# Optimization experiments

Hardware: AMD Instinct MI355X
Metric: run time of the kernel (lower is better)

Reference implementation:

```python
import jax, jax.numpy as jnp
import numpy as np

D_IN = 1024
D_OUT = 1024


def setup_inputs() -> dict:
    key = jax.random.key(0)
    ks = jax.random.split(key, 7)
    x = jax.random.normal(ks[0], (4, 2048, D_IN), dtype=jnp.float32)
    scale = 1.0 / np.sqrt(D_IN)
    Wq = jax.random.normal(ks[1], (D_IN, D_OUT), dtype=jnp.float32) * scale
    Wk = jax.random.normal(ks[2], (D_IN, D_OUT), dtype=jnp.float32) * scale
    Wv = jax.random.normal(ks[3], (D_IN, D_OUT), dtype=jnp.float32) * scale
    bq = jax.random.normal(ks[4], (D_OUT,), dtype=jnp.float32) * 0.01
    bk = jax.random.normal(ks[5], (D_OUT,), dtype=jnp.float32) * 0.01
    bv = jax.random.normal(ks[6], (D_OUT,), dtype=jnp.float32) * 0.01
    return {"x": x, "Wq": Wq, "bq": bq, "Wk": Wk, "bk": bk, "Wv": Wv, "bv": bv}


def reference(x, Wq, bq, Wk, bk, Wv, bv):
    # x: [B, S, d_in]
    q = jnp.einsum("bsd,de->bse", x, Wq) + bq  # [B, S, d_out]
    k = jnp.einsum("bsd,de->bse", x, Wk) + bk
    v = jnp.einsum("bsd,de->bse", x, Wv) + bv
    d_out = q.shape[-1]
    scores = jnp.einsum("bqe,bke->bqk", q, k) / jnp.sqrt(jnp.float32(d_out))
    attn = jax.nn.softmax(scores, axis=-1)  # [B, S, S]
    return jnp.einsum("bqk,bke->bqe", attn, v)
```

## Files before the change

### kernel.cpp

```cpp
#include <hip/hip_runtime.h>
#include <hip/hip_bf16.h>
#include <stdint.h>

typedef __bf16 bf16x8 __attribute__((ext_vector_type(8)));
typedef __bf16 bf16x4 __attribute__((ext_vector_type(4)));
typedef float f32x4 __attribute__((ext_vector_type(4)));

#define DEV __device__ __forceinline__

DEV void gload_lds16(const void* g, void* l) {
  __builtin_amdgcn_global_load_lds((const __attribute__((address_space(1))) void*)g,
                                   (__attribute__((address_space(3))) void*)l, 16, 0, 0);
}

#define WAITV(n) asm volatile("s_waitcnt vmcnt(" #n ")" ::: "memory")

__global__ __launch_bounds__(256) void pack_x_kernel(const float* __restrict__ x,
                                                     __bf16* __restrict__ o, long n) {
  long i = ((long)blockIdx.x * 256 + threadIdx.x) * 4;
  const long stride = (long)gridDim.x * 256 * 4;
  for (; i < n; i += stride) {
    f32x4 v = *(const f32x4*)(x + i);
    bf16x4 b;
    b[0] = (__bf16)v[0]; b[1] = (__bf16)v[1]; b[2] = (__bf16)v[2]; b[3] = (__bf16)v[3];
    *(bf16x4*)(o + i) = b;
  }
}

__global__ __launch_bounds__(256) void pack_w_kernel(const float* __restrict__ Wq,
                                                     const float* __restrict__ Wk,
                                                     const float* __restrict__ Wv,
                                                     __bf16* __restrict__ Wt) {
  const int w = blockIdx.z;
  const float* W = (w == 0) ? Wq : (w == 1) ? Wk : Wv;
  const float scale = (w == 0) ? 0.03125f : 1.0f;
  const int d0 = blockIdx.x * 64;
  const int e0 = blockIdx.y * 64;
  __shared__ __bf16 T[64][72];
  const int tid = threadIdx.x;
  const int r4 = tid >> 4;
  const int c4 = (tid & 15) * 4;
#pragma unroll
  for (int p = 0; p < 4; ++p) {
    int r = r4 + p * 16;
    f32x4 v = *(const f32x4*)(W + (long)(d0 + r) * 1024 + e0 + c4);
    T[r][c4 + 0] = (__bf16)(v[0] * scale);
    T[r][c4 + 1] = (__bf16)(v[1] * scale);
    T[r][c4 + 2] = (__bf16)(v[2] * scale);
    T[r][c4 + 3] = (__bf16)(v[3] * scale);
  }
  __syncthreads();
  const int e4 = tid >> 3;
  const int dd = (tid & 7) * 8;
#pragma unroll
  for (int p = 0; p < 2; ++p) {
    int e = e4 + p * 32;
    bf16x8 ov;
#pragma unroll
    for (int j = 0; j < 8; ++j) ov[j] = T[dd + j][e];
    *(bf16x8*)(Wt + (long)w * 1048576 + (long)(e0 + e) * 1024 + d0 + dd) = ov;
  }
}

__global__ __launch_bounds__(256) void pack_bias_kernel(const float* __restrict__ bq,
                                                        const float* __restrict__ bk,
                                                        const float* __restrict__ bv,
                                                        float* __restrict__ o) {
  int i = blockIdx.x * 256 + threadIdx.x;
  if (i < 1024) o[i] = bq[i] * 0.03125f;
  else if (i < 2048) o[i] = bk[i - 1024];
  else if (i < 3072) o[i] = bv[i - 2048];
}

template <int M_REP, int RING, bool OUT_BF16, bool BIAS>
__global__ __launch_bounds__(512, 2) void gemm256_kernel(
    const __bf16* __restrict__ A, int lda,
    const __bf16* __restrict__ B, int ldb, long long bBatchStride, int bmShift,
    const float* __restrict__ bias,
    void* __restrict__ C, int ldc,
    int nTiles, int nt) {
  constexpr int BM = M_REP * 32;
  constexpr int A_LOADS = BM / 64;
  constexpr int ABYTES = BM * 128;
  constexpr int BUFB = ABYTES + 32768;
  __shared__ __attribute__((aligned(128))) char lds[RING * BUFB];

  const int tid = threadIdx.x;
  const int lane = tid & 63;
  const int wid = tid >> 6;
  const int wm = wid >> 2, wn = wid & 3;
  const int lo = lane & 15, hi = lane >> 4;
  const int bm = blockIdx.x / nTiles, bn = blockIdx.x % nTiles;
  const __bf16* Bb = B + (long long)(bm >> bmShift) * bBatchStride;

  const __bf16* gA[A_LOADS]; int lA[A_LOADS];
  const __bf16* gB[4]; int lB[4];
#pragma unroll
  for (int l = 0; l < A_LOADS; ++l) {
    int s = l * 512 + tid, r = s >> 3;
    int c = (s & 7) ^ (r & 7);
    gA[l] = A + (long long)(bm * BM + r) * lda + c * 8;
    lA[l] = s * 16;
  }
#pragma unroll
  for (int l = 0; l < 4; ++l) {
    int s = l * 512 + tid, r = s >> 3;
    int c = (s & 7) ^ (r & 7);
    gB[l] = Bb + (long long)(bn * 256 + r) * ldb + c * 8;
    lB[l] = ABYTES + s * 16;
  }

  int aRow[M_REP], bRow[4];
  const int cx = ((hi ^ (lo & 7)) << 4);
#pragma unroll
  for (int mi = 0; mi < M_REP; ++mi)
    aRow[mi] = (wm * (M_REP * 16) + mi * 16 + lo) * 128;
#pragma unroll
  for (int ni = 0; ni < 4; ++ni)
    bRow[ni] = ABYTES + (wn * 64 + ni * 16 + lo) * 128;

#define STAGE(t, buf)                                                \
  do {                                                               \
    const long long ko_ = (long long)(t) * 64;                       \
    char* lb_ = lds + (buf) * BUFB;                                  \
    _Pragma("unroll") for (int l = 0; l < A_LOADS; ++l)              \
        gload_lds16(gA[l] + ko_, lb_ + lA[l]);                       \
    _Pragma("unroll") for (int l = 0; l < 4; ++l)                    \
        gload_lds16(gB[l] + ko_, lb_ + lB[l]);                       \
  } while (0)

  f32x4 acc[M_REP][4] = {};

  if constexpr (RING == 2) {
    STAGE(0, 0);
    WAITV(0);
  } else {
    STAGE(0, 0);
    STAGE(1, 1);
    WAITV(6);
  }
  __builtin_amdgcn_s_barrier();
  __builtin_amdgcn_sched_barrier(0);

  for (int t = 0; t < nt; ++t) {
    if constexpr (RING == 2) {
      if (t + 1 < nt) STAGE(t + 1, (t + 1) & 1);
    } else {
      if (t + 2 < nt) STAGE(t + 2, (t + 2) % 3);
    }
    const char* base = lds + (t % RING) * BUFB;

    {
      bf16x8 av[M_REP], bv[4];
#pragma unroll
      for (int mi = 0; mi < M_REP; ++mi) av[mi] = *(const bf16x8*)(base + aRow[mi] + cx);
#pragma unroll
      for (int ni = 0; ni < 4; ++ni) bv[ni] = *(const bf16x8*)(base + bRow[ni] + cx);
      __builtin_amdgcn_s_setprio(1);
#pragma unroll
      for (int mi = 0; mi < M_REP; ++mi)
#pragma unroll
        for (int ni = 0; ni < 4; ++ni)
          acc[mi][ni] = __builtin_amdgcn_mfma_f32_16x16x32_bf16(av[mi], bv[ni], acc[mi][ni], 0, 0, 0);
      __builtin_amdgcn_s_setprio(0);
    }
    __builtin_amdgcn_s_barrier();
    __builtin_amdgcn_sched_barrier(0);
    {
      bf16x8 av[M_REP], bv[4];
#pragma unroll
      for (int mi = 0; mi < M_REP; ++mi) av[mi] = *(const bf16x8*)(base + aRow[mi] + (cx ^ 64));
#pragma unroll
      for (int ni = 0; ni < 4; ++ni) bv[ni] = *(const bf16x8*)(base + bRow[ni] + (cx ^ 64));
      __builtin_amdgcn_s_setprio(1);
#pragma unroll
      for (int mi = 0; mi < M_REP; ++mi)
#pragma unroll
        for (int ni = 0; ni < 4; ++ni)
          acc[mi][ni] = __builtin_amdgcn_mfma_f32_16x16x32_bf16(av[mi], bv[ni], acc[mi][ni], 0, 0, 0);
      __builtin_amdgcn_s_setprio(0);
    }
    if (t + 1 < nt) {
      if constexpr (RING == 2) {
        WAITV(0);
      } else {
        if (t + 2 < nt) WAITV(6);
        else WAITV(0);
      }
      __builtin_amdgcn_s_barrier();
      __builtin_amdgcn_sched_barrier(0);
    }
  }
#undef STAGE

  char* Cb = (char*)C;
  const long long row0 = (long long)bm * BM + wm * (M_REP * 16) + hi * 4;
  const long long col0 = (long long)bn * 256 + wn * 64 + lo;
#pragma unroll
  for (int ni = 0; ni < 4; ++ni) {
    const long long col = col0 + ni * 16;
    const float bvs = BIAS ? bias[col] : 0.0f;
#pragma unroll
    for (int mi = 0; mi < M_REP; ++mi) {
#pragma unroll
      for (int j = 0; j < 4; ++j) {
        long long row = row0 + mi * 16 + j;
        float v = acc[mi][ni][j] + bvs;
        if (OUT_BF16)
          ((__bf16*)Cb)[row * ldc + col] = (__bf16)v;
        else
          ((float*)Cb)[row * ldc + col] = v;
      }
    }
  }
}

__global__ __launch_bounds__(256) void transpose_v_kernel(const __bf16* __restrict__ QKV,
                                                          __bf16* __restrict__ Vt) {
  const int t0 = blockIdx.x * 64;
  const int e0 = blockIdx.y * 64;
  const int b = blockIdx.z;
  __shared__ __bf16 T[64][72];
  const int tid = threadIdx.x;
  const int rr = tid >> 3;
  const int cc = (tid & 7) * 8;
  const __bf16* src = QKV + (long long)b * 2048 * 3072 + 2048;
#pragma unroll
  for (int p = 0; p < 2; ++p) {
    int t = rr + p * 32;
    bf16x8 v = *(const bf16x8*)(src + (long long)(t0 + t) * 3072 + e0 + cc);
#pragma unroll
    for (int j = 0; j < 8; ++j) T[t][cc + j] = v[j];
  }
  __syncthreads();
  __bf16* dst = Vt + (long long)b * 1024 * 2048;
#pragma unroll
  for (int p = 0; p < 2; ++p) {
    int e = rr + p * 32;
    bf16x8 ov;
#pragma unroll
    for (int j = 0; j < 8; ++j) ov[j] = T[cc + j][e];
    *(bf16x8*)(dst + (long long)(e0 + e) * 2048 + t0 + cc) = ov;
  }
}

__global__ __launch_bounds__(256) void softmax_kernel(float* __restrict__ S) {
  const long long row = blockIdx.x;
  float* p = S + row * 2048;
  const int tid = threadIdx.x;
  const int lane = tid & 63, wid = tid >> 6;
  f32x4 v0 = *(const f32x4*)(p + tid * 8);
  f32x4 v1 = *(const f32x4*)(p + tid * 8 + 4);
  float xv[8] = {v0[0], v0[1], v0[2], v0[3], v1[0], v1[1], v1[2], v1[3]};
  float mx = xv[0];
#pragma unroll
  for (int j = 1; j < 8; ++j) mx = fmaxf(mx, xv[j]);
#pragma unroll
  for (int off = 32; off >= 1; off >>= 1) mx = fmaxf(mx, __shfl_xor(mx, off));
  __shared__ float red[8];
  if (lane == 0) red[wid] = mx;
  __syncthreads();
  mx = fmaxf(fmaxf(red[0], red[1]), fmaxf(red[2], red[3]));
  float e[8];
  float sum = 0.f;
#pragma unroll
  for (int j = 0; j < 8; ++j) {
    e[j] = __expf(xv[j] - mx);
    sum += e[j];
  }
#pragma unroll
  for (int off = 32; off >= 1; off >>= 1) sum += __shfl_xor(sum, off);
  if (lane == 0) red[4 + wid] = sum;
  __syncthreads();
  sum = red[4] + red[5] + red[6] + red[7];
  const float inv = 1.0f / sum;
  bf16x8 ov;
#pragma unroll
  for (int j = 0; j < 8; ++j) ov[j] = (__bf16)(e[j] * inv);
  *(bf16x8*)((__bf16*)p + tid * 8) = ov;
}

extern "C" void kernel_launch(void* const* d_in, const int* in_sizes, int n_in,
                              void* d_out, int out_size, void* d_ws, size_t ws_size,
                              hipStream_t stream) {
  (void)in_sizes; (void)n_in; (void)out_size;
  const float* x  = (const float*)d_in[0];
  const float* Wq = (const float*)d_in[1];
  const float* bq = (const float*)d_in[2];
  const float* Wk = (const float*)d_in[3];
  const float* bk = (const float*)d_in[4];
  const float* Wv = (const float*)d_in[5];
  const float* bv = (const float*)d_in[6];
  float* out = (float*)d_out;
  char* ws = (char*)d_ws;
  if (ws_size < 157298688ULL) return;

  __bf16* x16  = (__bf16*)(ws + 0);
  __bf16* Wt   = (__bf16*)(ws + 16777216);
  float*  bqkv = (float*)(ws + 23068672);
  __bf16* QKV  = (__bf16*)(ws + 23080960);
  __bf16* Vt   = (__bf16*)(ws + 73412608);
  float*  S    = (float*)(ws + 90189824);

  pack_x_kernel<<<2048, 256, 0, stream>>>(x, x16, 8388608L);
  pack_w_kernel<<<dim3(16, 16, 3), 256, 0, stream>>>(Wq, Wk, Wv, Wt);
  pack_bias_kernel<<<12, 256, 0, stream>>>(bq, bk, bv, bqkv);

  gemm256_kernel<4, 3, true, true><<<dim3(64 * 12), 512, 0, stream>>>(
      x16, 1024, Wt, 1024, 0LL, 30, bqkv, QKV, 3072, 12, 16);

  gemm256_kernel<8, 2, false, false><<<dim3(32 * 8), 512, 0, stream>>>(
      QKV, 3072, QKV + 1024, 3072, 6291456LL, 3, nullptr, S, 2048, 8, 16);

  transpose_v_kernel<<<dim3(32, 16, 4), 256, 0, stream>>>(QKV, Vt);

  softmax_kernel<<<8192, 256, 0, stream>>>(S);

  gemm256_kernel<4, 3, false, false><<<dim3(64 * 4), 512, 0, stream>>>(
      (const __bf16*)S, 4096, Vt, 2048, 2097152LL, 4, nullptr, out, 1024, 4, 32);
}
```

Before: 192.0 us.

## Unify GEMMs on 256x256 tiles, fuse V transpose, split-K final GEMM

Replaces the templated GEMM with a single 256x256-tile kernel that uses a double buffer. Global-to-LDS loads for the next K tile are interleaved across four MFMA phases, and block indices are swizzled in groups of 8. The QKV projection now writes V directly in transposed layout, removing the separate transpose kernel. The attention-times-V GEMM is split along K into two partial fp32 outputs that an extra add kernel combines. This trades fewer launches and more in-flight blocks for extra partial-sum traffic and a larger register footprint per block.

```diff
diff --git a/kernel.cpp b/kernel.cpp
--- a/kernel.cpp
+++ b/kernel.cpp
@@ -14,6 +14,7 @@
 }
 
 #define WAITV(n) asm volatile("s_waitcnt vmcnt(" #n ")" ::: "memory")
+#define MFMA16x16(a, b, c) __builtin_amdgcn_mfma_f32_16x16x32_bf16(a, b, c, 0, 0, 0)
 
 __global__ __launch_bounds__(256) void pack_x_kernel(const float* __restrict__ x,
                                                      __bf16* __restrict__ o, long n) {
@@ -72,175 +73,171 @@
   else if (i < 3072) o[i] = bv[i - 2048];
 }
 
-template <int M_REP, int RING, bool OUT_BF16, bool BIAS>
-__global__ __launch_bounds__(512, 2) void gemm256_kernel(
+template <int MODE>
+__global__ __launch_bounds__(512, 2) void gemm_kernel(
     const __bf16* __restrict__ A, int lda,
     const __bf16* __restrict__ B, int ldb, long long bBatchStride, int bmShift,
     const float* __restrict__ bias,
     void* __restrict__ C, int ldc,
-    int nTiles, int nt) {
-  constexpr int BM = M_REP * 32;
-  constexpr int A_LOADS = BM / 64;
-  constexpr int ABYTES = BM * 128;
-  constexpr int BUFB = ABYTES + 32768;
-  __shared__ __attribute__((aligned(128))) char lds[RING * BUFB];
+    __bf16* __restrict__ vt,
+    int nTiles, int nt,
+    int khA, int khB, long long khCBytes) {
+  constexpr int ABYTES = 256 * 128;
+  constexpr int BUFB = ABYTES + 256 * 128;
+  __shared__ __attribute__((aligned(128))) char lds[2 * BUFB];
 
   const int tid = threadIdx.x;
   const int lane = tid & 63;
   const int wid = tid >> 6;
   const int wm = wid >> 2, wn = wid & 3;
   const int lo = lane & 15, hi = lane >> 4;
-  const int bm = blockIdx.x / nTiles, bn = blockIdx.x % nTiles;
-  const __bf16* Bb = B + (long long)(bm >> bmShift) * bBatchStride;
-
-  const __bf16* gA[A_LOADS]; int lA[A_LOADS];
+
+  const int cpx = gridDim.x >> 3;
+  const int bid = blockIdx.x;
+  const int swz = (bid & 7) * cpx + (bid >> 3);
+  const int bm = swz / nTiles, bn = swz % nTiles;
+  const int kh = blockIdx.y;
+
+  const __bf16* Ab = A + kh * khA;
+  const __bf16* Bb = B + (long long)(bm >> bmShift) * bBatchStride + kh * khB;
+
+  const __bf16* gA[4]; int lA[4];
   const __bf16* gB[4]; int lB[4];
-#pragma unroll
-  for (int l = 0; l < A_LOADS; ++l) {
-    int s = l * 512 + tid, r = s >> 3;
-    int c = (s & 7) ^ (r & 7);
-    gA[l] = A + (long long)(bm * BM + r) * lda + c * 8;
-    lA[l] = s * 16;
-  }
 #pragma unroll
   for (int l = 0; l < 4; ++l) {
     int s = l * 512 + tid, r = s >> 3;
     int c = (s & 7) ^ (r & 7);
+    gA[l] = Ab + (long long)(bm * 256 + r) * lda + c * 8;
+    lA[l] = s * 16;
     gB[l] = Bb + (long long)(bn * 256 + r) * ldb + c * 8;
     lB[l] = ABYTES + s * 16;
   }
 
-  int aRow[M_REP], bRow[4];
   const int cx = ((hi ^ (lo & 7)) << 4);
-#pragma unroll
-  for (int mi = 0; mi < M_REP; ++mi)
-    aRow[mi] = (wm * (M_REP * 16) + mi * 16 + lo) * 128;
-#pragma unroll
-  for (int ni = 0; ni < 4; ++ni)
-    bRow[ni] = ABYTES + (wn * 64 + ni * 16 + lo) * 128;
-
-#define STAGE(t, buf)                                                \
+  const int aR = wm * 128 + lo;
+  const int bR = wn * 64 + lo;
+
+  f32x4 acc[8][4] = {};
+  bf16x8 bv[4][2];
+
+#define STAGE_ALL(tt, buf)                                           \
   do {                                                               \
-    const long long ko_ = (long long)(t) * 64;                       \
+    const long long ko_ = (long long)(tt) * 64;                      \
     char* lb_ = lds + (buf) * BUFB;                                  \
-    _Pragma("unroll") for (int l = 0; l < A_LOADS; ++l)              \
-        gload_lds16(gA[l] + ko_, lb_ + lA[l]);                       \
-    _Pragma("unroll") for (int l = 0; l < 4; ++l)                    \
-        gload_lds16(gB[l] + ko_, lb_ + lB[l]);                       \
+    _Pragma("unroll") for (int l = 0; l < 4; ++l) {                  \
+      gload_lds16(gA[l] + ko_, lb_ + lA[l]);                         \
+      gload_lds16(gB[l] + ko_, lb_ + lB[l]);                         \
+    }                                                                \
   } while (0)
 
-  f32x4 acc[M_REP][4] = {};
-
-  if constexpr (RING == 2) {
-    STAGE(0, 0);
-    WAITV(0);
-  } else {
-    STAGE(0, 0);
-    STAGE(1, 1);
-    WAITV(6);
-  }
+#define PHASE(mi0, STG)                                                              \
+  {                                                                                  \
+    bf16x8 a00 = *(const bf16x8*)(base + (aR + (mi0) * 16) * 128 + cx);              \
+    bf16x8 a01 = *(const bf16x8*)(base + (aR + (mi0) * 16) * 128 + (cx ^ 64));       \
+    bf16x8 a10 = *(const bf16x8*)(base + (aR + (mi0) * 16 + 16) * 128 + cx);         \
+    bf16x8 a11 = *(const bf16x8*)(base + (aR + (mi0) * 16 + 16) * 128 + (cx ^ 64));  \
+    STG;                                                                             \
+    __builtin_amdgcn_s_setprio(1);                                                   \
+    _Pragma("unroll") for (int ni = 0; ni < 4; ++ni) {                               \
+      acc[(mi0)][ni] = MFMA16x16(a00, bv[ni][0], acc[(mi0)][ni]);                    \
+      acc[(mi0) + 1][ni] = MFMA16x16(a10, bv[ni][0], acc[(mi0) + 1][ni]);            \
+    }                                                                                \
+    _Pragma("unroll") for (int ni = 0; ni < 4; ++ni) {                               \
+      acc[(mi0)][ni] = MFMA16x16(a01, bv[ni][1], acc[(mi0)][ni]);                    \
+      acc[(mi0) + 1][ni] = MFMA16x16(a11, bv[ni][1], acc[(mi0) + 1][ni]);            \
+    }                                                                                \
+    __builtin_amdgcn_s_setprio(0);                                                   \
+  }
+
+  STAGE_ALL(0, 0);
+  WAITV(0);
   __builtin_amdgcn_s_barrier();
   __builtin_amdgcn_sched_barrier(0);
 
   for (int t = 0; t < nt; ++t) {
-    if constexpr (RING == 2) {
-      if (t + 1 < nt) STAGE(t + 1, (t + 1) & 1);
-    } else {
-      if (t + 2 < nt) STAGE(t + 2, (t + 2) % 3);
+    const char* base = lds + (t & 1) * BUFB;
+    char* sb = lds + ((t + 1) & 1) * BUFB;
+    const long long ko = (long long)(t + 1) * 64;
+    const bool st = (t + 1 < nt);
+
+#pragma unroll
+    for (int ni = 0; ni < 4; ++ni) {
+      bv[ni][0] = *(const bf16x8*)(base + (bR + ni * 16) * 128 + ABYTES + cx);
+      bv[ni][1] = *(const bf16x8*)(base + (bR + ni * 16) * 128 + ABYTES + (cx ^ 64));
     }
-    const char* base = lds + (t % RING) * BUFB;
-
-    {
-      bf16x8 av[M_REP], bv[4];
-#pragma unroll
-      for (int mi = 0; mi < M_REP; ++mi) av[mi] = *(const bf16x8*)(base + aRow[mi] + cx);
-#pragma unroll
-      for (int ni = 0; ni < 4; ++ni) bv[ni] = *(const bf16x8*)(base + bRow[ni] + cx);
-      __builtin_amdgcn_s_setprio(1);
-#pragma unroll
-      for (int mi = 0; mi < M_REP; ++mi)
-#pragma unroll
-        for (int ni = 0; ni < 4; ++ni)
-          acc[mi][ni] = __builtin_amdgcn_mfma_f32_16x16x32_bf16(av[mi], bv[ni], acc[mi][ni], 0, 0, 0);
-      __builtin_amdgcn_s_setprio(0);
-    }
+    PHASE(0, if (st) {
+      gload_lds16(gA[0] + ko, sb + lA[0]);
+      gload_lds16(gA[1] + ko, sb + lA[1]);
+      gload_lds16(gA[2] + ko, sb + lA[2]);
+    });
     __builtin_amdgcn_s_barrier();
-    __builtin_amdgcn_sched_barrier(0);
-    {
-      bf16x8 av[M_REP], bv[4];
-#pragma unroll
-      for (int mi = 0; mi < M_REP; ++mi) av[mi] = *(const bf16x8*)(base + aRow[mi] + (cx ^ 64));
-#pragma unroll
-      for (int ni = 0; ni < 4; ++ni) bv[ni] = *(const bf16x8*)(base + bRow[ni] + (cx ^ 64));
-      __builtin_amdgcn_s_setprio(1);
-#pragma unroll
-      for (int mi = 0; mi < M_REP; ++mi)
-#pragma unroll
-        for (int ni = 0; ni < 4; ++ni)
-          acc[mi][ni] = __builtin_amdgcn_mfma_f32_16x16x32_bf16(av[mi], bv[ni], acc[mi][ni], 0, 0, 0);
-      __builtin_amdgcn_s_setprio(0);
-    }
-    if (t + 1 < nt) {
-      if constexpr (RING == 2) {
-        WAITV(0);
-      } else {
-        if (t + 2 < nt) WAITV(6);
-        else WAITV(0);
-      }
+    PHASE(2, if (st) {
+      gload_lds16(gA[3] + ko, sb + lA[3]);
+      gload_lds16(gB[0] + ko, sb + lB[0]);
+      gload_lds16(gB[1] + ko, sb + lB[1]);
+    });
+    __builtin_amdgcn_s_barrier();
+    PHASE(4, if (st) {
+      gload_lds16(gB[2] + ko, sb + lB[2]);
+      gload_lds16(gB[3] + ko, sb + lB[3]);
+    });
+    __builtin_amdgcn_s_barrier();
+    PHASE(6, );
+
+    if (st) {
+      WAITV(0);
       __builtin_amdgcn_s_barrier();
       __builtin_amdgcn_sched_barrier(0);
     }
   }
-#undef STAGE
-
-  char* Cb = (char*)C;
-  const long long row0 = (long long)bm * BM + wm * (M_REP * 16) + hi * 4;
+#undef STAGE_ALL
+#undef PHASE
+
+  char* Cb = (char*)C + kh * khCBytes;
+  const long long row0 = (long long)bm * 256 + wm * 128 + hi * 4;
   const long long col0 = (long long)bn * 256 + wn * 64 + lo;
-#pragma unroll
-  for (int ni = 0; ni < 4; ++ni) {
-    const long long col = col0 + ni * 16;
-    const float bvs = BIAS ? bias[col] : 0.0f;
-#pragma unroll
-    for (int mi = 0; mi < M_REP; ++mi) {
-#pragma unroll
-      for (int j = 0; j < 4; ++j) {
-        long long row = row0 + mi * 16 + j;
-        float v = acc[mi][ni][j] + bvs;
-        if (OUT_BF16)
-          ((__bf16*)Cb)[row * ldc + col] = (__bf16)v;
-        else
-          ((float*)Cb)[row * ldc + col] = v;
+
+  if (MODE == 0) {
+#pragma unroll
+    for (int ni = 0; ni < 4; ++ni) {
+      const long long col = col0 + ni * 16;
+#pragma unroll
+      for (int mi = 0; mi < 8; ++mi) {
+#pragma unroll
+        for (int j = 0; j < 4; ++j)
+          ((float*)Cb)[(row0 + mi * 16 + j) * ldc + col] = acc[mi][ni][j];
       }
     }
-  }
-}
-
-__global__ __launch_bounds__(256) void transpose_v_kernel(const __bf16* __restrict__ QKV,
-                                                          __bf16* __restrict__ Vt) {
-  const int t0 = blockIdx.x * 64;
-  const int e0 = blockIdx.y * 64;
-  const int b = blockIdx.z;
-  __shared__ __bf16 T[64][72];
-  const int tid = threadIdx.x;
-  const int rr = tid >> 3;
-  const int cc = (tid & 7) * 8;
-  const __bf16* src = QKV + (long long)b * 2048 * 3072 + 2048;
-#pragma unroll
-  for (int p = 0; p < 2; ++p) {
-    int t = rr + p * 32;
-    bf16x8 v = *(const bf16x8*)(src + (long long)(t0 + t) * 3072 + e0 + cc);
-#pragma unroll
-    for (int j = 0; j < 8; ++j) T[t][cc + j] = v[j];
-  }
-  __syncthreads();
-  __bf16* dst = Vt + (long long)b * 1024 * 2048;
-#pragma unroll
-  for (int p = 0; p < 2; ++p) {
-    int e = rr + p * 32;
-    bf16x8 ov;
-#pragma unroll
-    for (int j = 0; j < 8; ++j) ov[j] = T[cc + j][e];
-    *(bf16x8*)(dst + (long long)(e0 + e) * 2048 + t0 + cc) = ov;
+  } else {
+    if (bn < 8) {
+#pragma unroll
+      for (int ni = 0; ni < 4; ++ni) {
+        const long long col = col0 + ni * 16;
+        const float bvs = bias[col];
+#pragma unroll
+        for (int mi = 0; mi < 8; ++mi) {
+#pragma unroll
+          for (int j = 0; j < 4; ++j)
+            ((__bf16*)Cb)[(row0 + mi * 16 + j) * ldc + col] = (__bf16)(acc[mi][ni][j] + bvs);
+        }
+      }
+    } else {
+      const int b = bm >> 3;
+      __bf16* vtb = vt + (long long)b * 2097152;
+      const int trow = (bm & 7) * 256 + wm * 128 + hi * 4;
+#pragma unroll
+      for (int ni = 0; ni < 4; ++ni) {
+        const long long e = (long long)(bn - 8) * 256 + wn * 64 + ni * 16 + lo;
+        const float bvs = bias[2048 + e];
+#pragma unroll
+        for (int mi = 0; mi < 8; ++mi) {
+          bf16x4 o;
+#pragma unroll
+          for (int j = 0; j < 4; ++j) o[j] = (__bf16)(acc[mi][ni][j] + bvs);
+          *(bf16x4*)(vtb + e * 2048 + trow + mi * 16) = o;
+        }
+      }
+    }
   }
 }
 
@@ -278,6 +275,18 @@
 #pragma unroll
   for (int j = 0; j < 8; ++j) ov[j] = (__bf16)(e[j] * inv);
   *(bf16x8*)((__bf16*)p + tid * 8) = ov;
+}
+
+__global__ __launch_bounds__(256) void add_kernel(const float* __restrict__ p0,
+                                                  const float* __restrict__ p1,
+                                                  float* __restrict__ o, long n) {
+  long i = ((long)blockIdx.x * 256 + threadIdx.x) * 4;
+  const long stride = (long)gridDim.x * 256 * 4;
+  for (; i < n; i += stride) {
+    f32x4 a = *(const f32x4*)(p0 + i);
+    f32x4 b = *(const f32x4*)(p1 + i);
+    *(f32x4*)(o + i) = a + b;
+  }
 }
 
 extern "C" void kernel_launch(void* const* d_in, const int* in_sizes, int n_in,
@@ -301,21 +310,24 @@
   __bf16* QKV  = (__bf16*)(ws + 23080960);
   __bf16* Vt   = (__bf16*)(ws + 73412608);
   float*  S    = (float*)(ws + 90189824);
+  float*  P0   = (float*)(ws + 0);
+  float*  P1   = (float*)(ws + 33554432);
 
   pack_x_kernel<<<2048, 256, 0, stream>>>(x, x16, 8388608L);
   pack_w_kernel<<<dim3(16, 16, 3), 256, 0, stream>>>(Wq, Wk, Wv, Wt);
   pack_bias_kernel<<<12, 256, 0, stream>>>(bq, bk, bv, bqkv);
 
-  gemm256_kernel<4, 3, true, true><<<dim3(64 * 12), 512, 0, stream>>>(
-      x16, 1024, Wt, 1024, 0LL, 30, bqkv, QKV, 3072, 12, 16);
-
-  gemm256_kernel<8, 2, false, false><<<dim3(32 * 8), 512, 0, stream>>>(
-      QKV, 3072, QKV + 1024, 3072, 6291456LL, 3, nullptr, S, 2048, 8, 16);
-
-  transpose_v_kernel<<<dim3(32, 16, 4), 256, 0, stream>>>(QKV, Vt);
+  gemm_kernel<1><<<dim3(384, 1), 512, 0, stream>>>(
+      x16, 1024, Wt, 1024, 0LL, 30, bqkv, QKV, 3072, Vt, 12, 16, 0, 0, 0LL);
+
+  gemm_kernel<0><<<dim3(256, 1), 512, 0, stream>>>(
+      QKV, 3072, QKV + 1024, 3072, 6291456LL, 3, nullptr, S, 2048, nullptr, 8, 16, 0, 0, 0LL);
 
   softmax_kernel<<<8192, 256, 0, stream>>>(S);
 
-  gemm256_kernel<4, 3, false, false><<<dim3(64 * 4), 512, 0, stream>>>(
-      (const __bf16*)S, 4096, Vt, 2048, 2097152LL, 4, nullptr, out, 1024, 4, 32);
-}
+  gemm_kernel<0><<<dim3(128, 2), 512, 0, stream>>>(
+      (const __bf16*)S, 4096, Vt, 2048, 2097152LL, 3, nullptr, P0, 1024, nullptr,
+      4, 16, 1024, 1024, 33554432LL);
+
+  add_kernel<<<2048, 256, 0, stream>>>(P0, P1, out, 8388608L);
+}
```

Result: slower. 198.0 us (+3.2%).
